# Kernel optimization log

Measured on AMD Instinct MI355X. Metric: run time of the kernel, lower is better.

## Reference

```python
import jax, jax.numpy as jnp
import numpy as np
from jax import lax

K = 3  # deform kernel size (forced by shape consistency of the offset branch)


def conv2d(x, w, b, pad):
    y = lax.conv_general_dilated(x, w, (1, 1), [(pad, pad), (pad, pad)],
                                 dimension_numbers=('NCHW', 'OIHW', 'NCHW'))
    return y + b[None, :, None, None]


def deform_conv(x, offset, w):
    # Deformable conv v1, stride 1, pad 0, per-group offsets, zero outside borders.
    B, Cin, H, W = x.shape
    Cout = w.shape[0]
    Ho, Wo = H - K + 1, W - K + 1
    G = offset.shape[1] // (2 * K * K)  # num deformable groups (= cin // c_p_g)
    cpg = Cin // G
    # offset layout: [B, G, K*K, 2(y,x), Ho, Wo]
    off = offset.reshape(B, G, K * K, 2, Ho, Wo)
    ky = (jnp.arange(K * K) // K).astype(x.dtype)
    kx = (jnp.arange(K * K) % K).astype(x.dtype)
    py = off[:, :, :, 0] + jnp.arange(Ho, dtype=x.dtype)[None, None, None, :, None] + ky[None, None, :, None, None]
    px = off[:, :, :, 1] + jnp.arange(Wo, dtype=x.dtype)[None, None, None, None, :] + kx[None, None, :, None, None]
    y0 = jnp.floor(py)
    x0 = jnp.floor(px)
    fy = (py - y0)[..., None]  # [B,G,KK,Ho,Wo,1]
    fx = (px - x0)[..., None]
    y0i = y0.astype(jnp.int32)
    x0i = x0.astype(jnp.int32)
    xr = x.reshape(B, G, cpg, H, W)
    bi = jnp.arange(B)[:, None, None, None, None]
    gi = jnp.arange(G)[None, :, None, None, None]

    def gather(iy, ix):
        valid = (iy >= 0) & (iy < H) & (ix >= 0) & (ix < W)
        v = xr[bi, gi, :, jnp.clip(iy, 0, H - 1), jnp.clip(ix, 0, W - 1)]  # [B,G,KK,Ho,Wo,cpg]
        return v * valid[..., None].astype(x.dtype)

    v = ((1 - fy) * (1 - fx) * gather(y0i, x0i)
         + (1 - fy) * fx * gather(y0i, x0i + 1)
         + fy * (1 - fx) * gather(y0i + 1, x0i)
         + fy * fx * gather(y0i + 1, x0i + 1))
    # [B,G,KK,Ho,Wo,cpg] -> [B, Cin*K*K, Ho, Wo] matching weight layout [Cout, Cin, K, K]
    cols = v.transpose(0, 1, 5, 2, 3, 4).reshape(B, Cin * K * K, Ho, Wo)
    return jnp.einsum('ok,bkhw->bohw', w.reshape(Cout, -1), cols)


def setup_inputs() -> dict:
    key = jax.random.key(0)
    ks = jax.random.split(key, 8)
    B, cin, cout, H, W = 4, 64, 64, 130, 130
    s = 0.05
    x = jax.random.normal(ks[0], (B, cin, H, W), jnp.float32)
    w0 = jax.random.normal(ks[1], (cin, cin, 3, 3), jnp.float32) * s
    b0 = jnp.zeros((cin,), jnp.float32)
    w1 = jax.random.normal(ks[2], (cin // 2, cin, 1, 1), jnp.float32) * s
    b1 = jnp.zeros((cin // 2,), jnp.float32)
    w2 = jax.random.normal(ks[3], (cin // 2, cin // 2, 3, 3), jnp.float32) * s
    b2 = jnp.zeros((cin // 2,), jnp.float32)
    off_ch = cin * 2 * K * K  # c_p_g = 1 -> G = cin
    w3 = jax.random.normal(ks[4], (off_ch, cin // 2, 1, 1), jnp.float32) * s
    b3 = jnp.zeros((off_ch,), jnp.float32)
    wd = jax.random.normal(ks[5], (cout, cin, K, K), jnp.float32) * s
    return {"x": x, "w0": w0, "b0": b0, "w1": w1, "b1": b1, "w2": w2, "b2": b2,
            "w3": w3, "b3": b3, "wd": wd}


def reference(x, w0, b0, w1, b1, w2, b2, w3, b3, wd):
    t = conv2d(x, w0, b0, 0)                                   # [B,cin,H-2,W-2]
    t = lax.reduce_window(t, -jnp.inf, lax.max, (1, 1, 2, 2), (1, 1, 2, 2), 'VALID')
    t = conv2d(t, w1, b1, 0)
    t = conv2d(t, w2, b2, 1)
    t = conv2d(t, w3, b3, 0)                                   # offset logits
    t = jnp.repeat(jnp.repeat(t, 2, axis=2), 2, axis=3)        # nearest x2 upsample
    return deform_conv(x, t, wd)
```

## Files before the change

kernel.cpp:

```cpp
#include <hip/hip_runtime.h>
#include <hip/hip_bf16.h>
#include <hip/hip_fp16.h>


#define HX 130
#define WX 130

typedef short bf16x8 __attribute__((ext_vector_type(8)));
typedef _Float16 f16x8 __attribute__((ext_vector_type(8)));
typedef float f32x4 __attribute__((ext_vector_type(4)));

static __device__ __forceinline__ unsigned short f2bf(float f) {
    unsigned u = __float_as_uint(f);
    unsigned r = u + 0x7fff + ((u >> 16) & 1);
    return (unsigned short)(r >> 16);
}

static __device__ __forceinline__ int aoff320(int row, int col) {
    return row * 320 + ((((col >> 3) ^ (row & 7))) << 3) + (col & 7);
}

static __device__ __forceinline__ int aoff192(int row, int col) {
    return row * 192 + ((((col >> 3) ^ (row & 7))) << 3) + (col & 7);
}

__global__ __launch_bounds__(256) void k_wdt(const float* __restrict__ wd,
                                             const float* __restrict__ w3,
                                             const float* __restrict__ w0,
                                             unsigned short* __restrict__ wdtb,
                                             __half* __restrict__ w3h,
                                             unsigned short* __restrict__ w0b) {
    int idx = blockIdx.x * 256 + threadIdx.x;
    if (idx < 36864) {
        int o = idx / 576;
        int rem = idx - o * 576;
        int c = rem / 9;
        int kk = rem - c * 9;
        int h = c >> 5;
        int c5 = c & 31;
        int col = (c5 >> 4) * 144 + ((c5 >> 3) & 1) * 72 + (c5 & 7) * 9 + kk;
        wdtb[(size_t)(h * 64 + o) * 288 + col] = f2bf(wd[idx]);
        if (idx < 16) wdtb[36864 + idx] = 0;
    } else if (idx < 73728) {
        int i2 = idx - 36864;
        w3h[i2] = __float2half_rn(w3[i2]);
    } else {
        int i3 = idx - 73728;
        int row = i3 / 160;
        int col = i3 - row * 160;
        int cig = row >> 6, oc = row & 63;
        unsigned short v = 0;
        if (col < 144) {
            int ci = (col * 57) >> 9;
            int kk = col - ci * 9;
            v = f2bf(w0[(size_t)(oc * 64 + cig * 16 + ci) * 9 + kk]);
        }
        w0b[i3] = v;
    }
}

__global__ __launch_bounds__(256, 4) void k_conv0_mfma(const float* __restrict__ x,
                                                       const unsigned short* __restrict__ w0b,
                                                       const float* __restrict__ b0,
                                                       float* __restrict__ p1) {
    int blk = blockIdx.x;
    int tx = blk & 15;
    int ty = (blk >> 4) & 15;
    int b = blk >> 8;
    int tid = threadIdx.x;
    int w = tid >> 6;
    int lane = tid & 63;
    int lm = lane & 15;
    int lq = lane >> 4;
    int oy0 = ty * 8, ox0 = tx * 8;

    __shared__ __align__(16) unsigned short alds[64 * 192];
    __shared__ __align__(16) float xlds[1600];

    f32x4 acc[4];
    #pragma unroll
    for (int n = 0; n < 4; ++n) acc[n] = (f32x4){0.f, 0.f, 0.f, 0.f};

    if (tid < 128) {
        *(bf16x8*)&alds[aoff192(tid >> 1, 144 + (tid & 1) * 8)] =
            (bf16x8){0, 0, 0, 0, 0, 0, 0, 0};
    }

    const float* xb = x + (size_t)(b * 64) * (HX * WX) + oy0 * WX + ox0;
    int apx = tid >> 2;
    int acq = tid & 3;
    int py = apx >> 3, pxx = apx & 7;

    for (int cig = 0; cig < 4; ++cig) {
        #pragma unroll
        for (int j = 0; j < 7; ++j) {
            int i = tid + j * 256;
            if (i < 1600) {
                int ci = i / 100;
                int rem = i - ci * 100;
                int rr = rem / 10, cc = rem - rr * 10;
                xlds[i] = xb[(size_t)(cig * 16 + ci) * (HX * WX) + rr * WX + cc];
            }
        }
        __syncthreads();
        #pragma unroll
        for (int jj = 0; jj < 36; ++jj) {
            int col = acq * 36 + jj;
            int ci = (col * 57) >> 9;
            int kk = col - ci * 9;
            int ky = kk / 3, kx = kk - ky * 3;
            alds[aoff192(apx, col)] =
                f2bf(xlds[ci * 100 + (py + ky) * 10 + (pxx + kx)]);
        }
        __syncthreads();
        int arow = w * 16 + lm;
        const unsigned short* bbase = w0b + (size_t)cig * 64 * 160;
        #pragma unroll
        for (int ks = 0; ks < 5; ++ks) {
            bf16x8 a = *(const bf16x8*)&alds[aoff192(arow, ks * 32 + lq * 8)];
            #pragma unroll
            for (int n = 0; n < 4; ++n) {
                bf16x8 bb = *(const bf16x8*)(bbase + (size_t)(n * 16 + lm) * 160
                                             + ks * 32 + lq * 8);
                acc[n] = __builtin_amdgcn_mfma_f32_16x16x32_bf16(a, bb, acc[n], 0, 0, 0);
            }
        }
    }

    __syncthreads();
    float* dlds = (float*)alds;
    #pragma unroll
    for (int n = 0; n < 4; ++n) {
        int oc = n * 16 + lm;
        #pragma unroll
        for (int r = 0; r < 4; ++r) {
            int px = w * 16 + lq * 4 + r;
            dlds[oc * 65 + px] = acc[n][r];
        }
    }
    __syncthreads();
    {
        int oc = tid >> 2;
        int ppy = tid & 3;
        float bo = b0[oc];
        float4 o4;
        #pragma unroll
        for (int ppx = 0; ppx < 4; ++ppx) {
            const float* dp = &dlds[oc * 65 + (2 * ppy) * 8 + 2 * ppx];
            float m = fmaxf(fmaxf(dp[0], dp[1]), fmaxf(dp[8], dp[9])) + bo;
            ((float*)&o4)[ppx] = m;
        }
        *(float4*)(p1 + (((size_t)b * 64 + oc) * 64 + ty * 4 + ppy) * 64 + tx * 4) = o4;
    }
}

__global__ __launch_bounds__(256) void k_conv1x1_a(const float* __restrict__ p1,
                                                   const float* __restrict__ w1,
                                                   const float* __restrict__ b1,
                                                   float* __restrict__ t2) {
    int blk = blockIdx.x;
    int pt = blk & 15;
    int cog = (blk >> 4) & 15;
    int b = blk >> 8;
    int p = pt * 256 + threadIdx.x;
    float acc[2];
    #pragma unroll
    for (int i = 0; i < 2; ++i) acc[i] = b1[cog * 2 + i];
    const float* ip = p1 + (size_t)b * 64 * 4096 + p;
    for (int ci = 0; ci < 64; ++ci) {
        float v = ip[(size_t)ci * 4096];
        #pragma unroll
        for (int i = 0; i < 2; ++i) acc[i] += w1[(cog * 2 + i) * 64 + ci] * v;
    }
    float* op = t2 + (size_t)b * 32 * 4096 + p;
    #pragma unroll
    for (int i = 0; i < 2; ++i) op[(size_t)(cog * 2 + i) * 4096] = acc[i];
}

__global__ __launch_bounds__(256) void k_conv3x3_b(const float* __restrict__ t2,
                                                   const float* __restrict__ w2,
                                                   const float* __restrict__ b2,
                                                   float* __restrict__ t3) {
    int blk = blockIdx.x;
    int pt = blk & 15;
    int cog = (blk >> 4) & 15;
    int b = blk >> 8;
    int p = pt * 256 + threadIdx.x;
    int hy = p >> 6, wx = p & 63;
    float acc[2];
    #pragma unroll
    for (int i = 0; i < 2; ++i) acc[i] = b2[cog * 2 + i];
    const float* ip = t2 + (size_t)b * 32 * 4096;
    for (int ci = 0; ci < 32; ++ci) {
        float v[9];
        #pragma unroll
        for (int ky = 0; ky < 3; ++ky) {
            int yy = hy + ky - 1;
            #pragma unroll
            for (int kx = 0; kx < 3; ++kx) {
                int xx = wx + kx - 1;
                bool ok = (yy >= 0 && yy < 64 && xx >= 0 && xx < 64);
                int yc = min(max(yy, 0), 63), xc = min(max(xx, 0), 63);
                float val = ip[(size_t)ci * 4096 + yc * 64 + xc];
                v[ky * 3 + kx] = ok ? val : 0.f;
            }
        }
        #pragma unroll
        for (int i = 0; i < 2; ++i) {
            const float* wp = w2 + (((cog * 2 + i) * 32) + ci) * 9;
            float s = acc[i];
            #pragma unroll
            for (int k = 0; k < 9; ++k) s += wp[k] * v[k];
            acc[i] = s;
        }
    }
    float* op = t3 + (size_t)b * 32 * 4096 + p;
    #pragma unroll
    for (int i = 0; i < 2; ++i) op[(size_t)(cog * 2 + i) * 4096] = acc[i];
}

__global__ __launch_bounds__(256, 3) void k_deform(const float* __restrict__ x,
                                                   const float* __restrict__ t3,
                                                   const __half* __restrict__ w3h,
                                                   const float* __restrict__ b3,
                                                   const unsigned short* __restrict__ wdtb,
                                                   float* __restrict__ out) {
    int blk = blockIdx.x;
    int b = blk & 3;
    int strip = blk >> 2;
    int tid = threadIdx.x;
    int po0 = strip * 16;
    int qy = po0 >> 6;
    int qx0 = po0 & 63;
    int w = tid >> 6;
    int lane = tid & 63;
    int lm = lane & 15;
    int lq = lane >> 4;
    int tq = tid & 15;
    int kb = tid >> 4;

    __shared__ __align__(16) unsigned short alds[64 * 320];
    __shared__ __align__(16) __half2 soff[2304];
    __shared__ __align__(16) _Float16 st3t[16 * 40];

    f32x4 acc[4];
    #pragma unroll
    for (int n = 0; n < 4; ++n) acc[n] = (f32x4){0.f, 0.f, 0.f, 0.f};

    const float* xb = x + (size_t)b * 64 * HX * WX;
    float fybase = (float)(2 * qy);
    float fxbase = (float)(2 * (qx0 + tq));

    {
        int px = tid & 15, ci0 = tid >> 4;
        const float* t3p = t3 + (size_t)b * 32 * 4096 + (qy * 64 + qx0 + px);
        st3t[px * 40 + ci0]      = (_Float16)t3p[(size_t)ci0 * 4096];
        st3t[px * 40 + ci0 + 16] = (_Float16)t3p[(size_t)(ci0 + 16) * 4096];
    }
    __syncthreads();
    const f16x8 bfrag = *(const f16x8*)&st3t[lm * 40 + lq * 8];

    for (int h = 0; h < 2; ++h) {
        #pragma unroll 1
        for (int sl = 0; sl < 2; ++sl) {
            int s = h * 2 + sl;
            __syncthreads();

            #pragma unroll
            for (int rep = 0; rep < 5; ++rep) {
                int t = rep * 4 + w;
                if (rep == 4) { if (w >= 2) break; t = 16 + w; }
                const f16x8 afrag = *(const f16x8*)((const _Float16*)w3h
                        + (size_t)(s * 288 + t * 16 + lm) * 32 + lq * 8);
                f32x4 d = __builtin_amdgcn_mfma_f32_16x16x32_f16(
                        afrag, bfrag, (f32x4){0.f, 0.f, 0.f, 0.f}, 0, 0, 0);
                float4 bq = *(const float4*)(b3 + s * 288 + t * 16 + lq * 4);
                int p0 = (t * 8 + lq * 2) * 16 + lm;
                soff[p0]      = __floats2half2_rn(d[0] + bq.x, d[1] + bq.y);
                soff[p0 + 16] = __floats2half2_rn(d[2] + bq.z, d[3] + bq.w);
            }
            __syncthreads();

            __half2 o2h[9];
            #pragma unroll
            for (int it = 0; it < 9; ++it)
                o2h[it] = soff[it * 256 + tid];
            #pragma unroll
            for (int it = 0; it < 9; ++it) {
                int kcol = it * 16 + kb;
                int lc = kcol >= 72;
                int ckk = kcol - 72 * lc;
                int ch = (ckk * 57) >> 9;
                int kk = ckk - ch * 9;
                int c = s * 16 + lc * 8 + ch;
                int clocal = sl * 144 + kcol;
                float2 off = __half22float2(o2h[it]);
                float py = off.x + fybase + (float)(kk / 3);
                float px = off.y + fxbase + (float)(kk % 3);
                float y0f = floorf(py), x0f = floorf(px);
                float fy = py - y0f, fx = px - x0f;
                int y0 = (int)y0f, x0 = (int)x0f;
                const float* xp = xb + (size_t)c * (HX * WX);
                float tv[3][3];
                bool fastok = (y0 >= 0) & (y0 <= HX - 3) & (x0 >= 0) & (x0 <= WX - 3);
                if (__all(fastok)) {
                    int xe = x0 & ~1;
                    int odd = x0 & 1;
                    const float* rp = xp + y0 * WX + xe;
                    #pragma unroll
                    for (int r = 0; r < 3; ++r) {
                        float2 A = *(const float2*)(rp);
                        float2 B = *(const float2*)(rp + 2);
                        tv[r][0] = odd ? A.y : A.x;
                        tv[r][1] = odd ? B.x : A.y;
                        tv[r][2] = odd ? B.y : B.x;
                        rp += WX;
                    }
                } else {
                    #pragma unroll
                    for (int r = 0; r < 3; ++r) {
                        int yy = y0 + r;
                        bool vy = (yy >= 0) & (yy < HX);
                        int yc = min(max(yy, 0), HX - 1);
                        #pragma unroll
                        for (int sx = 0; sx < 3; ++sx) {
                            int xx = x0 + sx;
                            bool vx = (xx >= 0) & (xx < WX);
                            int xc = min(max(xx, 0), WX - 1);
                            float val = xp[yc * WX + xc];
                            tv[r][sx] = (vy & vx) ? val : 0.f;
                        }
                    }
                }
                float h0[3], h1[3];
                #pragma unroll
                for (int r = 0; r < 3; ++r) {
                    h0[r] = tv[r][0] + fx * (tv[r][1] - tv[r][0]);
                    h1[r] = tv[r][1] + fx * (tv[r][2] - tv[r][1]);
                }
                alds[aoff320(0 * 16 + tq, clocal)] = f2bf(h0[0] + fy * (h0[1] - h0[0]));
                alds[aoff320(1 * 16 + tq, clocal)] = f2bf(h1[0] + fy * (h1[1] - h1[0]));
                alds[aoff320(2 * 16 + tq, clocal)] = f2bf(h0[1] + fy * (h0[2] - h0[1]));
                alds[aoff320(3 * 16 + tq, clocal)] = f2bf(h1[1] + fy * (h1[2] - h1[1]));
            }
        }
        __syncthreads();

        int arow = w * 16 + lm;
        const unsigned short* bbase = wdtb + (size_t)(h * 64) * 288;
        #pragma unroll
        for (int ks = 0; ks < 9; ++ks) {
            bf16x8 a = *(const bf16x8*)&alds[aoff320(arow, ks * 32 + lq * 8)];
            #pragma unroll
            for (int n = 0; n < 4; ++n) {
                bf16x8 bb = *(const bf16x8*)(bbase + (size_t)(n * 16 + lm) * 288
                                             + ks * 32 + lq * 8);
                acc[n] = __builtin_amdgcn_mfma_f32_16x16x32_bf16(a, bb, acc[n], 0, 0, 0);
            }
        }
    }

    __syncthreads();
    float* dlds = (float*)alds;
    #pragma unroll
    for (int n = 0; n < 4; ++n) {
        int oc = n * 16 + lm;
        #pragma unroll
        for (int r = 0; r < 4; ++r) {
            int px = w * 16 + lq * 4 + r;
            dlds[oc * 65 + px] = acc[n][r];
        }
    }
    __syncthreads();
    {
        int oc = tid >> 2;
        int sy = (tid >> 1) & 1;
        int qh = (tid & 1) * 8;
        float* orow = out + (((size_t)b * 64 + oc) * 128 + 2 * qy + sy) * 128 + 2 * qx0;
        const float* d0 = &dlds[oc * 65 + (sy * 2 + 0) * 16];
        const float* d1 = &dlds[oc * 65 + (sy * 2 + 1) * 16];
        #pragma unroll
        for (int i = 0; i < 8; ++i) {
            int q = qh + i;
            *(float2*)(orow + 2 * q) = make_float2(d0[q], d1[q]);
        }
    }
}

extern "C" void kernel_launch(void* const* d_in, const int* in_sizes, int n_in,
                              void* d_out, int out_size, void* d_ws, size_t ws_size,
                              hipStream_t stream) {
    const float* x  = (const float*)d_in[0];
    const float* w0 = (const float*)d_in[1];
    const float* b0 = (const float*)d_in[2];
    const float* w1 = (const float*)d_in[3];
    const float* b1 = (const float*)d_in[4];
    const float* w2 = (const float*)d_in[5];
    const float* b2 = (const float*)d_in[6];
    const float* w3 = (const float*)d_in[7];
    const float* b3 = (const float*)d_in[8];
    const float* wd = (const float*)d_in[9];
    float* out = (float*)d_out;

    float* ws = (float*)d_ws;
    float* p1    = ws;
    float* t2    = p1 + 1048576;
    float* t3    = t2 + 524288;
    unsigned short* wdtb = (unsigned short*)(t3 + 524288);
    __half* w3h = (__half*)(wdtb + 36880);
    unsigned short* w0b = (unsigned short*)(w3h + 36864);

    k_wdt<<<448, 256, 0, stream>>>(wd, w3, w0, wdtb, w3h, w0b);
    k_conv0_mfma<<<1024, 256, 0, stream>>>(x, w0b, b0, p1);
    k_conv1x1_a<<<1024, 256, 0, stream>>>(p1, w1, b1, t2);
    k_conv3x3_b<<<1024, 256, 0, stream>>>(t2, w2, b2, t3);
    k_deform<<<1024, 256, 0, stream>>>(x, t3, w3h, b3, wdtb, out);
}
```

Before: 226.8 us.

## Move 3x3 offset-branch conv to bf16 MFMA and vectorize 1x1 conv

Replaces the scalar FP32 3x3 conv (t2->t3) with an MFMA kernel. It stages a padded 10x10 input tile per channel group in LDS, builds a swizzled bf16 im2col A tile, and multiplies it against bf16 pre-packed w2 weights produced in the weight-prep kernel. The 1x1 conv now processes four pixels per thread with float4 loads and stores, using a quarter of the blocks. This cuts scalar FMA and global-load cost in the offset branch, at the price of bf16 rounding of the offset logits, which can shift the sampling positions slightly.

```diff
diff --git a/kernel.cpp b/kernel.cpp
--- a/kernel.cpp
+++ b/kernel.cpp
@@ -27,9 +27,11 @@
 __global__ __launch_bounds__(256) void k_wdt(const float* __restrict__ wd,
                                              const float* __restrict__ w3,
                                              const float* __restrict__ w0,
+                                             const float* __restrict__ w2,
                                              unsigned short* __restrict__ wdtb,
                                              __half* __restrict__ w3h,
-                                             unsigned short* __restrict__ w0b) {
+                                             unsigned short* __restrict__ w0b,
+                                             unsigned short* __restrict__ w2b) {
     int idx = blockIdx.x * 256 + threadIdx.x;
     if (idx < 36864) {
         int o = idx / 576;
@@ -44,7 +46,7 @@
     } else if (idx < 73728) {
         int i2 = idx - 36864;
         w3h[i2] = __float2half_rn(w3[i2]);
-    } else {
+    } else if (idx < 114688) {
         int i3 = idx - 73728;
         int row = i3 / 160;
         int col = i3 - row * 160;
@@ -56,6 +58,18 @@
             v = f2bf(w0[(size_t)(oc * 64 + cig * 16 + ci) * 9 + kk]);
         }
         w0b[i3] = v;
+    } else {
+        int i4 = idx - 114688;
+        int row = i4 / 160;
+        int col = i4 - row * 160;
+        int cig = row >> 5, oc = row & 31;
+        unsigned short v = 0;
+        if (col < 144) {
+            int ci = (col * 57) >> 9;
+            int kk = col - ci * 9;
+            v = f2bf(w2[(size_t)(oc * 32 + cig * 16 + ci) * 9 + kk]);
+        }
+        w2b[i4] = v;
     }
 }
 
@@ -159,64 +173,126 @@
                                                    const float* __restrict__ b1,
                                                    float* __restrict__ t2) {
     int blk = blockIdx.x;
-    int pt = blk & 15;
-    int cog = (blk >> 4) & 15;
-    int b = blk >> 8;
-    int p = pt * 256 + threadIdx.x;
-    float acc[2];
-    #pragma unroll
-    for (int i = 0; i < 2; ++i) acc[i] = b1[cog * 2 + i];
-    const float* ip = p1 + (size_t)b * 64 * 4096 + p;
+    int qt = blk & 3;
+    int cog = (blk >> 2) & 15;
+    int b = blk >> 6;
+    int q = qt * 256 + threadIdx.x;
+    float4 acc[2];
+    #pragma unroll
+    for (int i = 0; i < 2; ++i) {
+        float bv = b1[cog * 2 + i];
+        acc[i] = make_float4(bv, bv, bv, bv);
+    }
+    const float* ip = p1 + (size_t)b * 64 * 4096 + q * 4;
     for (int ci = 0; ci < 64; ++ci) {
-        float v = ip[(size_t)ci * 4096];
-        #pragma unroll
-        for (int i = 0; i < 2; ++i) acc[i] += w1[(cog * 2 + i) * 64 + ci] * v;
-    }
-    float* op = t2 + (size_t)b * 32 * 4096 + p;
-    #pragma unroll
-    for (int i = 0; i < 2; ++i) op[(size_t)(cog * 2 + i) * 4096] = acc[i];
-}
-
-__global__ __launch_bounds__(256) void k_conv3x3_b(const float* __restrict__ t2,
-                                                   const float* __restrict__ w2,
-                                                   const float* __restrict__ b2,
-                                                   float* __restrict__ t3) {
+        float4 v = *(const float4*)(ip + (size_t)ci * 4096);
+        #pragma unroll
+        for (int i = 0; i < 2; ++i) {
+            float wv = w1[(cog * 2 + i) * 64 + ci];
+            acc[i].x += wv * v.x; acc[i].y += wv * v.y;
+            acc[i].z += wv * v.z; acc[i].w += wv * v.w;
+        }
+    }
+    float* op = t2 + (size_t)b * 32 * 4096 + q * 4;
+    #pragma unroll
+    for (int i = 0; i < 2; ++i)
+        *(float4*)(op + (size_t)(cog * 2 + i) * 4096) = acc[i];
+}
+
+__global__ __launch_bounds__(256, 4) void k_conv3_mfma(const float* __restrict__ t2,
+                                                       const unsigned short* __restrict__ w2b,
+                                                       const float* __restrict__ b2,
+                                                       float* __restrict__ t3) {
     int blk = blockIdx.x;
-    int pt = blk & 15;
-    int cog = (blk >> 4) & 15;
-    int b = blk >> 8;
-    int p = pt * 256 + threadIdx.x;
-    int hy = p >> 6, wx = p & 63;
-    float acc[2];
-    #pragma unroll
-    for (int i = 0; i < 2; ++i) acc[i] = b2[cog * 2 + i];
-    const float* ip = t2 + (size_t)b * 32 * 4096;
-    for (int ci = 0; ci < 32; ++ci) {
-        float v[9];
-        #pragma unroll
-        for (int ky = 0; ky < 3; ++ky) {
-            int yy = hy + ky - 1;
-            #pragma unroll
-            for (int kx = 0; kx < 3; ++kx) {
-                int xx = wx + kx - 1;
-                bool ok = (yy >= 0 && yy < 64 && xx >= 0 && xx < 64);
-                int yc = min(max(yy, 0), 63), xc = min(max(xx, 0), 63);
-                float val = ip[(size_t)ci * 4096 + yc * 64 + xc];
-                v[ky * 3 + kx] = ok ? val : 0.f;
-            }
-        }
-        #pragma unroll
-        for (int i = 0; i < 2; ++i) {
-            const float* wp = w2 + (((cog * 2 + i) * 32) + ci) * 9;
-            float s = acc[i];
-            #pragma unroll
-            for (int k = 0; k < 9; ++k) s += wp[k] * v[k];
-            acc[i] = s;
-        }
-    }
-    float* op = t3 + (size_t)b * 32 * 4096 + p;
-    #pragma unroll
-    for (int i = 0; i < 2; ++i) op[(size_t)(cog * 2 + i) * 4096] = acc[i];
+    int tx = blk & 7;
+    int ty = (blk >> 3) & 7;
+    int b = blk >> 6;
+    int tid = threadIdx.x;
+    int w = tid >> 6;
+    int lane = tid & 63;
+    int lm = lane & 15;
+    int lq = lane >> 4;
+    int oy0 = ty * 8, ox0 = tx * 8;
+
+    __shared__ __align__(16) unsigned short alds[64 * 192];
+    __shared__ __align__(16) float xlds[1600];
+
+    f32x4 acc[2];
+    #pragma unroll
+    for (int n = 0; n < 2; ++n) acc[n] = (f32x4){0.f, 0.f, 0.f, 0.f};
+
+    if (tid < 128) {
+        *(bf16x8*)&alds[aoff192(tid >> 1, 144 + (tid & 1) * 8)] =
+            (bf16x8){0, 0, 0, 0, 0, 0, 0, 0};
+    }
+
+    const float* tb = t2 + (size_t)(b * 32) * 4096;
+    int apx = tid >> 2;
+    int acq = tid & 3;
+    int py = apx >> 3, pxx = apx & 7;
+
+    for (int cig = 0; cig < 2; ++cig) {
+        #pragma unroll
+        for (int j = 0; j < 7; ++j) {
+            int i = tid + j * 256;
+            if (i < 1600) {
+                int ci = i / 100;
+                int rem = i - ci * 100;
+                int rr = rem / 10, cc = rem - rr * 10;
+                int gy = oy0 + rr - 1, gx = ox0 + cc - 1;
+                bool ok = (gy >= 0) & (gy < 64) & (gx >= 0) & (gx < 64);
+                xlds[i] = ok ? tb[(size_t)(cig * 16 + ci) * 4096 + gy * 64 + gx]
+                             : 0.f;
+            }
+        }
+        __syncthreads();
+        #pragma unroll
+        for (int jj = 0; jj < 36; ++jj) {
+            int col = acq * 36 + jj;
+            int ci = (col * 57) >> 9;
+            int kk = col - ci * 9;
+            int ky = kk / 3, kx = kk - ky * 3;
+            alds[aoff192(apx, col)] =
+                f2bf(xlds[ci * 100 + (py + ky) * 10 + (pxx + kx)]);
+        }
+        __syncthreads();
+        int arow = w * 16 + lm;
+        const unsigned short* bbase = w2b + (size_t)cig * 32 * 160;
+        #pragma unroll
+        for (int ks = 0; ks < 5; ++ks) {
+            bf16x8 a = *(const bf16x8*)&alds[aoff192(arow, ks * 32 + lq * 8)];
+            #pragma unroll
+            for (int n = 0; n < 2; ++n) {
+                bf16x8 bb = *(const bf16x8*)(bbase + (size_t)(n * 16 + lm) * 160
+                                             + ks * 32 + lq * 8);
+                acc[n] = __builtin_amdgcn_mfma_f32_16x16x32_bf16(a, bb, acc[n], 0, 0, 0);
+            }
+        }
+    }
+
+    __syncthreads();
+    float* dlds = (float*)alds;
+    #pragma unroll
+    for (int n = 0; n < 2; ++n) {
+        int oc = n * 16 + lm;
+        #pragma unroll
+        for (int r = 0; r < 4; ++r) {
+            int px = w * 16 + lq * 4 + r;
+            dlds[oc * 65 + px] = acc[n][r];
+        }
+    }
+    __syncthreads();
+    {
+        int oc = tid >> 3;
+        int r = tid & 7;
+        float bo = b2[oc];
+        const float* dp = &dlds[oc * 65 + r * 8];
+        float* op = t3 + ((size_t)(b * 32 + oc) * 64 + oy0 + r) * 64 + ox0;
+        float4 a4 = make_float4(dp[0] + bo, dp[1] + bo, dp[2] + bo, dp[3] + bo);
+        float4 b4 = make_float4(dp[4] + bo, dp[5] + bo, dp[6] + bo, dp[7] + bo);
+        *(float4*)(op) = a4;
+        *(float4*)(op + 4) = b4;
+    }
 }
 
 __global__ __launch_bounds__(256, 3) void k_deform(const float* __restrict__ x,
@@ -409,10 +485,11 @@
     unsigned short* wdtb = (unsigned short*)(t3 + 524288);
     __half* w3h = (__half*)(wdtb + 36880);
     unsigned short* w0b = (unsigned short*)(w3h + 36864);
-
-    k_wdt<<<448, 256, 0, stream>>>(wd, w3, w0, wdtb, w3h, w0b);
+    unsigned short* w2b = w0b + 40960;
+
+    k_wdt<<<488, 256, 0, stream>>>(wd, w3, w0, w2, wdtb, w3h, w0b, w2b);
     k_conv0_mfma<<<1024, 256, 0, stream>>>(x, w0b, b0, p1);
-    k_conv1x1_a<<<1024, 256, 0, stream>>>(p1, w1, b1, t2);
-    k_conv3x3_b<<<1024, 256, 0, stream>>>(t2, w2, b2, t3);
+    k_conv1x1_a<<<256, 256, 0, stream>>>(p1, w1, b1, t2);
+    k_conv3_mfma<<<256, 256, 0, stream>>>(t2, w2b, b2, t3);
     k_deform<<<1024, 256, 0, stream>>>(x, t3, w3h, b3, wdtb, out);
 }
```

After: 223.5 us. No clear change (-1.4%).
